# Kernel tuning notes

Measured on AMD Instinct MI355X. Metric: run time of the kernel, lower is better.

Reference implementation:

```python
import jax, jax.numpy as jnp
import numpy as np


def setup_inputs() -> dict:
    key = jax.random.key(0)
    k1, k2, k3, k4 = jax.random.split(key, 4)
    B, L, F, V = 512, 512, 64, 20000
    src_ids = jax.random.randint(k1, (B, L), 0, V, dtype=jnp.int32)
    dst_ids = jax.random.randint(k2, (B, L), 0, V, dtype=jnp.int32)
    # MLP params: Linear(1->F), ReLU, Linear(F->F)
    W1 = jax.random.normal(k3, (1, F), dtype=jnp.float32)  # fan_in = 1
    b1 = jnp.zeros((F,), dtype=jnp.float32)
    W2 = jax.random.normal(k4, (F, F), dtype=jnp.float32) * (1.0 / np.sqrt(F))
    b2 = jnp.zeros((F,), dtype=jnp.float32)
    return {"src_ids": src_ids, "dst_ids": dst_ids, "W1": W1, "b1": b1,
            "W2": W2, "b2": b2, "num_nodes": V}


def reference(src_ids, dst_ids, W1, b1, W2, b2, num_nodes):
    # Per-row histogram over node ids (vectorized replacement for
    # np.unique + dict gather in the torch code).
    row_hist = lambda r: jnp.bincount(r, length=num_nodes)
    hist_src = jax.vmap(row_hist)(src_ids)  # [B, V]
    hist_dst = jax.vmap(row_hist)(dst_ids)  # [B, V]

    gather = lambda h, ids: jnp.take_along_axis(h, ids, axis=1)  # [B, L]

    # appearances: [count in own seq, count in other seq], shape [B, L, 2]
    src_app = jnp.stack([gather(hist_src, src_ids), gather(hist_dst, src_ids)], axis=-1).astype(jnp.float32)
    dst_app = jnp.stack([gather(hist_src, dst_ids), gather(hist_dst, dst_ids)], axis=-1).astype(jnp.float32)
    # id 0 is padding -> zero both count channels
    src_app = jnp.where((src_ids == 0)[..., None], 0.0, src_app)
    dst_app = jnp.where((dst_ids == 0)[..., None], 0.0, dst_app)

    def encode(app):
        # app: [B, L, 2]; per-scalar MLP then sum over the 2 count channels
        h = jax.nn.relu(app[..., None] * W1[0] + b1)  # [B, L, 2, F]
        out = h @ W2 + b2                              # [B, L, 2, F]
        return out.sum(axis=2)                         # [B, L, F]

    return encode(src_app), encode(dst_app)
```

## Files before the change

kernel.cpp:

```cpp
#include <hip/hip_runtime.h>

constexpr int Bn = 512;
constexpr int Ln = 512;
constexpr int Fn = 64;
constexpr int Vn = 20000;
constexpr int HWORDS = (Vn + 2) / 3;
constexpr int BL = Bn * Ln;

__global__ void build_table_kernel(const float* __restrict__ W1,
                                   const float* __restrict__ b1,
                                   const float* __restrict__ W2,
                                   const float* __restrict__ b2,
                                   float* __restrict__ table) {
    const int v = blockIdx.x;
    const int j = threadIdx.x;
    __shared__ float h[Fn];
    h[j] = fmaxf((float)v * W1[j] + b1[j], 0.0f);
    __syncthreads();
    float acc = b2[j];
#pragma unroll
    for (int i = 0; i < Fn; ++i)
        acc = fmaf(h[i], W2[i * Fn + j], acc);
    table[v * Fn + j] = acc;
}

__device__ __forceinline__ unsigned hist_get(const unsigned* __restrict__ h, int v) {
    const int w = v / 3;
    const int f = v - w * 3;
    return (h[w] >> (10 * f)) & 0x3FFu;
}

__global__ __launch_bounds__(256) void hist_kernel(
    const int* __restrict__ src_ids,
    const int* __restrict__ dst_ids,
    unsigned* __restrict__ counts) {
    __shared__ unsigned hs[HWORDS];
    __shared__ unsigned hd[HWORDS];

    const int b = blockIdx.x;
    const int tid = threadIdx.x;

    for (int i = tid; i < HWORDS; i += 256) { hs[i] = 0u; hd[i] = 0u; }
    __syncthreads();

    const int* __restrict__ srow = src_ids + b * Ln;
    const int* __restrict__ drow = dst_ids + b * Ln;

    const int s0 = srow[tid], s1 = srow[tid + 256];
    const int d0 = drow[tid], d1 = drow[tid + 256];
    {
        int w;
        w = s0 / 3; atomicAdd(&hs[w], 1u << (10 * (s0 - w * 3)));
        w = s1 / 3; atomicAdd(&hs[w], 1u << (10 * (s1 - w * 3)));
        w = d0 / 3; atomicAdd(&hd[w], 1u << (10 * (d0 - w * 3)));
        w = d1 / 3; atomicAdd(&hd[w], 1u << (10 * (d1 - w * 3)));
    }
    __syncthreads();

    const size_t base = (size_t)b * Ln;
#pragma unroll
    for (int k = 0; k < 2; ++k) {
        const int l = tid + k * 256;
        const int s = (k == 0) ? s0 : s1;
        const int d = (k == 0) ? d0 : d1;
        unsigned ws = 0u, wd = 0u;
        if (s != 0) ws = hist_get(hs, s) | (hist_get(hd, s) << 16);
        if (d != 0) wd = hist_get(hs, d) | (hist_get(hd, d) << 16);
        counts[base + l] = ws;
        counts[BL + base + l] = wd;
    }
}

__global__ __launch_bounds__(256) void expand_kernel(
    const unsigned* __restrict__ counts,
    const float* __restrict__ table,
    float* __restrict__ out) {
    const unsigned g = blockIdx.x * 256u + threadIdx.x;
    const unsigned r = g & 15u;
    const unsigned idx = g >> 4;
    const unsigned w = counts[idx];
    const unsigned c0 = w & 0xFFFFu;
    const unsigned c1 = w >> 16;
    const float4 t0 = *((const float4*)(table + c0 * Fn) + r);
    const float4 t1 = *((const float4*)(table + c1 * Fn) + r);
    float4 o;
    o.x = t0.x + t1.x; o.y = t0.y + t1.y; o.z = t0.z + t1.z; o.w = t0.w + t1.w;
    *((float4*)(out + (size_t)idx * Fn) + r) = o;
}

extern "C" void kernel_launch(void* const* d_in, const int* in_sizes, int n_in,
                              void* d_out, int out_size, void* d_ws, size_t ws_size,
                              hipStream_t stream) {
    const int*   src_ids = (const int*)d_in[0];
    const int*   dst_ids = (const int*)d_in[1];
    const float* W1      = (const float*)d_in[2];
    const float* b1      = (const float*)d_in[3];
    const float* W2      = (const float*)d_in[4];
    const float* b2      = (const float*)d_in[5];

    float*    table  = (float*)d_ws;
    unsigned* counts = (unsigned*)(table + 513 * Fn);

    build_table_kernel<<<Ln + 1, Fn, 0, stream>>>(W1, b1, W2, b2, table);
    hist_kernel<<<Bn, 256, 0, stream>>>(src_ids, dst_ids, counts);
    expand_kernel<<<(2 * BL * 16) / 256, 256, 0, stream>>>(counts, table, (float*)d_out);
}
```

Measured before the change: 149.0 us.

## Fuse histogram and table-expand kernels into one per-row kernel with nontemporal stores

Merges the histogram kernel and the expand kernel into one kernel with one 512-thread block per batch row. Packed counts stay in shared memory instead of going through a global scratch buffer, and the output is written with nontemporal vector stores. This removes one launch and the counts round trip to global memory. In exchange there are only 512 blocks, each using more LDS, so occupancy and latency hiding during the large output-write phase may suffer.

```diff
diff --git a/kernel.cpp b/kernel.cpp
--- a/kernel.cpp
+++ b/kernel.cpp
@@ -6,6 +6,8 @@
 constexpr int Vn = 20000;
 constexpr int HWORDS = (Vn + 2) / 3;
 constexpr int BL = Bn * Ln;
+
+typedef float f32x4 __attribute__((ext_vector_type(4)));
 
 __global__ void build_table_kernel(const float* __restrict__ W1,
                                    const float* __restrict__ b1,
@@ -30,62 +32,57 @@
     return (h[w] >> (10 * f)) & 0x3FFu;
 }
 
-__global__ __launch_bounds__(256) void hist_kernel(
+__global__ __launch_bounds__(512) void fused_kernel(
     const int* __restrict__ src_ids,
     const int* __restrict__ dst_ids,
-    unsigned* __restrict__ counts) {
+    const float* __restrict__ table,
+    float* __restrict__ out) {
     __shared__ unsigned hs[HWORDS];
     __shared__ unsigned hd[HWORDS];
+    __shared__ unsigned pc[2 * Ln];
 
     const int b = blockIdx.x;
     const int tid = threadIdx.x;
 
-    for (int i = tid; i < HWORDS; i += 256) { hs[i] = 0u; hd[i] = 0u; }
+    for (int i = tid; i < HWORDS; i += 512) { hs[i] = 0u; hd[i] = 0u; }
     __syncthreads();
 
-    const int* __restrict__ srow = src_ids + b * Ln;
-    const int* __restrict__ drow = dst_ids + b * Ln;
-
-    const int s0 = srow[tid], s1 = srow[tid + 256];
-    const int d0 = drow[tid], d1 = drow[tid + 256];
+    const int s = src_ids[b * Ln + tid];
+    const int d = dst_ids[b * Ln + tid];
     {
         int w;
-        w = s0 / 3; atomicAdd(&hs[w], 1u << (10 * (s0 - w * 3)));
-        w = s1 / 3; atomicAdd(&hs[w], 1u << (10 * (s1 - w * 3)));
-        w = d0 / 3; atomicAdd(&hd[w], 1u << (10 * (d0 - w * 3)));
-        w = d1 / 3; atomicAdd(&hd[w], 1u << (10 * (d1 - w * 3)));
+        w = s / 3; atomicAdd(&hs[w], 1u << (10 * (s - w * 3)));
+        w = d / 3; atomicAdd(&hd[w], 1u << (10 * (d - w * 3)));
     }
     __syncthreads();
 
-    const size_t base = (size_t)b * Ln;
-#pragma unroll
-    for (int k = 0; k < 2; ++k) {
-        const int l = tid + k * 256;
-        const int s = (k == 0) ? s0 : s1;
-        const int d = (k == 0) ? d0 : d1;
+    {
         unsigned ws = 0u, wd = 0u;
         if (s != 0) ws = hist_get(hs, s) | (hist_get(hd, s) << 16);
         if (d != 0) wd = hist_get(hs, d) | (hist_get(hd, d) << 16);
-        counts[base + l] = ws;
-        counts[BL + base + l] = wd;
+        pc[tid] = ws;
+        pc[Ln + tid] = wd;
     }
-}
+    __syncthreads();
 
-__global__ __launch_bounds__(256) void expand_kernel(
-    const unsigned* __restrict__ counts,
-    const float* __restrict__ table,
-    float* __restrict__ out) {
-    const unsigned g = blockIdx.x * 256u + threadIdx.x;
-    const unsigned r = g & 15u;
-    const unsigned idx = g >> 4;
-    const unsigned w = counts[idx];
-    const unsigned c0 = w & 0xFFFFu;
-    const unsigned c1 = w >> 16;
-    const float4 t0 = *((const float4*)(table + c0 * Fn) + r);
-    const float4 t1 = *((const float4*)(table + c1 * Fn) + r);
-    float4 o;
-    o.x = t0.x + t1.x; o.y = t0.y + t1.y; o.z = t0.z + t1.z; o.w = t0.w + t1.w;
-    *((float4*)(out + (size_t)idx * Fn) + r) = o;
+    const f32x4* __restrict__ t4 = (const f32x4*)table;
+    f32x4* __restrict__ out4 = (f32x4*)out;
+    const size_t row0 = (size_t)b * Ln;
+#pragma unroll 4
+    for (int it = 0; it < 32; ++it) {
+        const unsigned g = (unsigned)it * 512u + tid;
+        const unsigned r = g & 15u;
+        const unsigned idx = g >> 4;
+        const unsigned a = idx >> 9;
+        const unsigned l = idx & 511u;
+        const unsigned wrd = pc[idx];
+        const unsigned c0 = wrd & 0xFFFFu;
+        const unsigned c1 = wrd >> 16;
+        const f32x4 t0 = t4[c0 * 16u + r];
+        const f32x4 t1 = t4[c1 * 16u + r];
+        const f32x4 o = t0 + t1;
+        __builtin_nontemporal_store(o, &out4[((size_t)a * BL + row0 + l) * 16u + r]);
+    }
 }
 
 extern "C" void kernel_launch(void* const* d_in, const int* in_sizes, int n_in,
@@ -98,10 +95,8 @@
     const float* W2      = (const float*)d_in[4];
     const float* b2      = (const float*)d_in[5];
 
-    float*    table  = (float*)d_ws;
-    unsigned* counts = (unsigned*)(table + 513 * Fn);
+    float* table = (float*)d_ws;
 
     build_table_kernel<<<Ln + 1, Fn, 0, stream>>>(W1, b1, W2, b2, table);
-    hist_kernel<<<Bn, 256, 0, stream>>>(src_ids, dst_ids, counts);
-    expand_kernel<<<(2 * BL * 16) / 256, 256, 0, stream>>>(counts, table, (float*)d_out);
+    fused_kernel<<<Bn, 512, 0, stream>>>(src_ids, dst_ids, table, (float*)d_out);
 }
```

Measured after the change: 154.8 us. 1.04x slower.

## Fuse table build into histogram kernel and grid-stride the expand kernel

Applied to the files above, without the earlier changes.

The separate MLP lookup-table kernel is folded into the histogram kernel: each block computes one table row, and the last block also computes row 512. This removes one launch. The expand kernel now uses a fixed grid of 4096 blocks, each thread handling 8 float4 outputs, so far fewer blocks are launched. The risk is that each thread now recomputes the hidden activations inline instead of reading them from shared memory, and the smaller grid may expose less memory parallelism.

```diff
diff --git a/kernel.cpp b/kernel.cpp
--- a/kernel.cpp
+++ b/kernel.cpp
@@ -7,22 +7,7 @@
 constexpr int HWORDS = (Vn + 2) / 3;
 constexpr int BL = Bn * Ln;
 
-__global__ void build_table_kernel(const float* __restrict__ W1,
-                                   const float* __restrict__ b1,
-                                   const float* __restrict__ W2,
-                                   const float* __restrict__ b2,
-                                   float* __restrict__ table) {
-    const int v = blockIdx.x;
-    const int j = threadIdx.x;
-    __shared__ float h[Fn];
-    h[j] = fmaxf((float)v * W1[j] + b1[j], 0.0f);
-    __syncthreads();
-    float acc = b2[j];
-#pragma unroll
-    for (int i = 0; i < Fn; ++i)
-        acc = fmaf(h[i], W2[i * Fn + j], acc);
-    table[v * Fn + j] = acc;
-}
+typedef float f32x4 __attribute__((ext_vector_type(4)));
 
 __device__ __forceinline__ unsigned hist_get(const unsigned* __restrict__ h, int v) {
     const int w = v / 3;
@@ -30,9 +15,14 @@
     return (h[w] >> (10 * f)) & 0x3FFu;
 }
 
-__global__ __launch_bounds__(256) void hist_kernel(
+__global__ __launch_bounds__(256) void prep_kernel(
     const int* __restrict__ src_ids,
     const int* __restrict__ dst_ids,
+    const float* __restrict__ W1,
+    const float* __restrict__ b1,
+    const float* __restrict__ W2,
+    const float* __restrict__ b2,
+    float* __restrict__ table,
     unsigned* __restrict__ counts) {
     __shared__ unsigned hs[HWORDS];
     __shared__ unsigned hd[HWORDS];
@@ -41,6 +31,29 @@
     const int tid = threadIdx.x;
 
     for (int i = tid; i < HWORDS; i += 256) { hs[i] = 0u; hd[i] = 0u; }
+
+    if (tid < Fn) {
+        const int j = tid;
+        const float v = (float)b;
+        float acc = b2[j];
+#pragma unroll
+        for (int i = 0; i < Fn; ++i) {
+            const float h = fmaxf(fmaf(v, W1[i], b1[i]), 0.0f);
+            acc = fmaf(h, W2[i * Fn + j], acc);
+        }
+        table[b * Fn + j] = acc;
+    }
+    if (b == Bn - 1 && tid >= 64 && tid < 64 + Fn) {
+        const int j = tid - 64;
+        const float v = (float)Ln;
+        float acc = b2[j];
+#pragma unroll
+        for (int i = 0; i < Fn; ++i) {
+            const float h = fmaxf(fmaf(v, W1[i], b1[i]), 0.0f);
+            acc = fmaf(h, W2[i * Fn + j], acc);
+        }
+        table[Ln * Fn + j] = acc;
+    }
     __syncthreads();
 
     const int* __restrict__ srow = src_ids + b * Ln;
@@ -75,17 +88,20 @@
     const unsigned* __restrict__ counts,
     const float* __restrict__ table,
     float* __restrict__ out) {
-    const unsigned g = blockIdx.x * 256u + threadIdx.x;
-    const unsigned r = g & 15u;
-    const unsigned idx = g >> 4;
-    const unsigned w = counts[idx];
-    const unsigned c0 = w & 0xFFFFu;
-    const unsigned c1 = w >> 16;
-    const float4 t0 = *((const float4*)(table + c0 * Fn) + r);
-    const float4 t1 = *((const float4*)(table + c1 * Fn) + r);
-    float4 o;
-    o.x = t0.x + t1.x; o.y = t0.y + t1.y; o.z = t0.z + t1.z; o.w = t0.w + t1.w;
-    *((float4*)(out + (size_t)idx * Fn) + r) = o;
+    const unsigned t = blockIdx.x * 256u + threadIdx.x;
+    const f32x4* __restrict__ t4 = (const f32x4*)table;
+    f32x4* __restrict__ out4 = (f32x4*)out;
+#pragma unroll
+    for (int it = 0; it < 8; ++it) {
+        const unsigned g = t + (unsigned)it * (4096u * 256u);
+        const unsigned r = g & 15u;
+        const unsigned idx = g >> 4;
+        const unsigned w = counts[idx];
+        const unsigned c0 = w & 0xFFFFu;
+        const unsigned c1 = w >> 16;
+        const f32x4 o = t4[c0 * 16u + r] + t4[c1 * 16u + r];
+        out4[g] = o;
+    }
 }
 
 extern "C" void kernel_launch(void* const* d_in, const int* in_sizes, int n_in,
@@ -101,7 +117,7 @@
     float*    table  = (float*)d_ws;
     unsigned* counts = (unsigned*)(table + 513 * Fn);
 
-    build_table_kernel<<<Ln + 1, Fn, 0, stream>>>(W1, b1, W2, b2, table);
-    hist_kernel<<<Bn, 256, 0, stream>>>(src_ids, dst_ids, counts);
-    expand_kernel<<<(2 * BL * 16) / 256, 256, 0, stream>>>(counts, table, (float*)d_out);
+    prep_kernel<<<Bn, 256, 0, stream>>>(src_ids, dst_ids, W1, b1, W2, b2,
+                                        table, counts);
+    expand_kernel<<<4096, 256, 0, stream>>>(counts, table, (float*)d_out);
 }
```

Measured after the change: 152.4 us. 2.3% more time.
